# Kernel tuning notes

Measured on AMD Instinct MI355X. Metric: run time of the kernel, lower is better.

## Reference

```python
import jax, jax.numpy as jnp
import numpy as np

N_NODES = 100000
N_EDGES = 500000
IN_FEATS = 128
HID = 128
OUT = 1


def setup_inputs() -> dict:
    key = jax.random.key(0)
    ks = jax.random.split(key, 10)
    h = jax.random.normal(ks[0], (N_NODES, IN_FEATS), dtype=jnp.float32)
    src = jax.random.randint(ks[1], (N_EDGES,), 0, N_NODES, dtype=jnp.int32)
    dst = jax.random.randint(ks[2], (N_EDGES,), 0, N_NODES, dtype=jnp.int32)
    # Linear params (PyTorch convention: W [out,in], y = x @ W.T + b)
    s1 = 1.0 / np.sqrt(2 * IN_FEATS)
    s2 = 1.0 / np.sqrt(HID)
    W1 = jax.random.uniform(ks[3], (HID, 2 * IN_FEATS), jnp.float32, -s1, s1)
    b1 = jax.random.uniform(ks[4], (HID,), jnp.float32, -s1, s1)
    W2 = jax.random.uniform(ks[5], (HID, HID), jnp.float32, -s2, s2)
    b2 = jax.random.uniform(ks[6], (HID,), jnp.float32, -s2, s2)
    W3 = jax.random.uniform(ks[7], (OUT, HID), jnp.float32, -s2, s2)
    b3 = jax.random.uniform(ks[8], (OUT,), jnp.float32, -s2, s2)
    return {"h": h, "src": src, "dst": dst,
            "W1": W1, "b1": b1, "W2": W2, "b2": b2, "W3": W3, "b3": b3}


def reference(h, src, dst, W1, b1, W2, b2, W3, b3):
    # Per-edge gather of src/dst node features. Instead of materializing the
    # [E, 2*in] concat, split W1 into its src/dst halves and fuse the concat
    # into two GEMMs (same math as fc1(cat([h_u, h_v], 1))).
    h_u = h[src]                                   # [E, in]
    h_v = h[dst]                                   # [E, in]
    W1u, W1v = W1[:, :IN_FEATS], W1[:, IN_FEATS:]  # [hid, in] each
    x = h_u @ W1u.T + h_v @ W1v.T + b1             # [E, hid]
    x = jax.nn.relu(x)
    x = jax.nn.relu(x @ W2.T + b2)                 # [E, hid]
    score = x @ W3.T + b3                          # [E, out]
    return score
```

## Files before the change

### kernel.cpp

```cpp
#include <hip/hip_runtime.h>
#include <hip/hip_bf16.h>
#include <hip/hip_fp16.h>


#define N_NODES 100000
#define N_EDGES 500000
#define F       128
#define HID     128
#define TE      32
#define NT      (N_EDGES / TE)
#define GRID    1024
#define BLOCK   256

typedef _Float16 f16x8  __attribute__((ext_vector_type(8)));
typedef float    f32x16 __attribute__((ext_vector_type(16)));

typedef __attribute__((address_space(3))) unsigned int  lds_u32;
typedef __attribute__((address_space(1))) const unsigned int glb_u32;

__device__ __forceinline__ void load_lds16(const void* g, void* l) {
    __builtin_amdgcn_global_load_lds((glb_u32*)g, (lds_u32*)l, 16, 0, 0);
}
__device__ __forceinline__ void bar_lgkm() {
    asm volatile("s_waitcnt lgkmcnt(0)" ::: "memory");
    __builtin_amdgcn_s_barrier();
    __builtin_amdgcn_sched_barrier(0);
}
__device__ __forceinline__ void bar_vm() {
    asm volatile("s_waitcnt vmcnt(0) lgkmcnt(0)" ::: "memory");
    __builtin_amdgcn_s_barrier();
    __builtin_amdgcn_sched_barrier(0);
}

__global__ __launch_bounds__(256) void h_to_f16(const float* __restrict__ h,
                                                _Float16* __restrict__ h16) {
    const int i = (blockIdx.x * 256 + threadIdx.x) * 8;
    float4 a = *(const float4*)(h + i);
    float4 b = *(const float4*)(h + i + 4);
    f16x8 v;
    v[0] = (_Float16)a.x; v[1] = (_Float16)a.y; v[2] = (_Float16)a.z; v[3] = (_Float16)a.w;
    v[4] = (_Float16)b.x; v[5] = (_Float16)b.y; v[6] = (_Float16)b.z; v[7] = (_Float16)b.w;
    *(f16x8*)(h16 + i) = v;
}

__global__ __launch_bounds__(BLOCK) void edge_mlp_v4(
    const _Float16* __restrict__ h16,
    const int*   __restrict__ src,
    const int*   __restrict__ dst,
    const float* __restrict__ W1,
    const float* __restrict__ b1,
    const float* __restrict__ W2,
    const float* __restrict__ b2,
    const float* __restrict__ W3,
    const float* __restrict__ b3,
    float*       __restrict__ out)
{
    __shared__ __align__(128) char Alds[2 * TE * 512];
    __shared__ __align__(128) char Xlds[TE * 256];
    float* Spart = (float*)Xlds;

    const int tid  = threadIdx.x;
    const int wave = tid >> 6;
    const int lane = tid & 63;
    const int mh   = wave;
    const int col  = lane & 31;
    const int h    = lane >> 5;

    f16x8 w1a[16];
    #pragma unroll
    for (int kt = 0; kt < 16; ++kt) {
        const float* p = W1 + (mh * 32 + col) * 256 + kt * 16 + 8 * h;
        f16x8 v;
        #pragma unroll
        for (int j = 0; j < 8; ++j) v[j] = (_Float16)p[j];
        w1a[kt] = v;
    }
    f16x8 w2a[8];
    #pragma unroll
    for (int kt = 0; kt < 8; ++kt) {
        const float* p = W2 + (mh * 32 + col) * 128 + kt * 16 + 8 * h;
        f16x8 v;
        #pragma unroll
        for (int j = 0; j < 8; ++j) v[j] = (_Float16)p[j];
        w2a[kt] = v;
    }
    float b1pl[16], b2pl[16], w3pl[16];
    #pragma unroll
    for (int r = 0; r < 16; ++r) {
        const int row = mh * 32 + (r & 3) + 8 * (r >> 2) + 4 * h;
        b1pl[r] = b1[row];
        b2pl[r] = b2[row];
        w3pl[r] = W3[row];
    }
    const float b3v = b3[0];

    int eloc[4], k16v[4];
    #pragma unroll
    for (int j = 0; j < 4; ++j) {
        const int i = wave * 4 + j;
        eloc[j] = 2 * i + h;
        k16v[j] = (lane & 15) ^ (eloc[j] & 15);
    }
    const int whichv = (lane >> 4) & 1;
    const int* idxp  = whichv ? dst : src;

    const int t0 = blockIdx.x;
    int nodeCur[4], nodeNext[4];

    #pragma unroll
    for (int j = 0; j < 4; ++j) {
        nodeCur[j] = idxp[t0 * TE + eloc[j]];
    }
    #pragma unroll
    for (int j = 0; j < 4; ++j) {
        const _Float16* g = h16 + (size_t)nodeCur[j] * F + k16v[j] * 8;
        load_lds16(g, Alds + (wave * 4 + j) * 1024);
    }
    {
        int tn = t0 + GRID; if (tn > NT - 1) tn = NT - 1;
        #pragma unroll
        for (int j = 0; j < 4; ++j) nodeNext[j] = idxp[tn * TE + eloc[j]];
    }

    const int e_own = col;
    const int exor  = (e_own & 15) << 4;

    int cur = 0;
    for (int t = t0; t < NT; t += GRID) {
        bar_vm();

        #pragma unroll
        for (int j = 0; j < 4; ++j) nodeCur[j] = nodeNext[j];
        {
            char* nb = Alds + (cur ^ 1) * (TE * 512);
            #pragma unroll
            for (int j = 0; j < 4; ++j) {
                const _Float16* g = h16 + (size_t)nodeCur[j] * F + k16v[j] * 8;
                load_lds16(g, nb + (wave * 4 + j) * 1024);
            }
        }
        {
            int tn2 = t + 2 * GRID; if (tn2 > NT - 1) tn2 = NT - 1;
            #pragma unroll
            for (int j = 0; j < 4; ++j) nodeNext[j] = idxp[tn2 * TE + eloc[j]];
        }

        const char* Ab = Alds + cur * (TE * 512);

        f32x16 acc1 = {};
        #pragma unroll
        for (int kt = 0; kt < 16; ++kt) {
            const int c = (kt * 32 + 16 * h) ^ exor;
            f16x8 bf = *(const f16x8*)(Ab + e_own * 512 + c);
            acc1 = __builtin_amdgcn_mfma_f32_32x32x16_f16(w1a[kt], bf, acc1, 0, 0, 0);
        }
        #pragma unroll
        for (int g = 0; g < 4; ++g) {
            union { _Float16 q[4]; unsigned long long u; } pk;
            #pragma unroll
            for (int q = 0; q < 4; ++q) {
                float v = acc1[4 * g + q] + b1pl[4 * g + q];
                v = v > 0.f ? v : 0.f;
                pk.q[q] = (_Float16)v;
            }
            const int c = (mh * 64 + 16 * g + 8 * h) ^ exor;
            *(unsigned long long*)(Xlds + e_own * 256 + c) = pk.u;
        }
        bar_lgkm();

        f32x16 acc2 = {};
        #pragma unroll
        for (int kt = 0; kt < 8; ++kt) {
            const int c = (kt * 32 + 16 * h) ^ exor;
            f16x8 xf = *(const f16x8*)(Xlds + e_own * 256 + c);
            acc2 = __builtin_amdgcn_mfma_f32_32x32x16_f16(w2a[kt], xf, acc2, 0, 0, 0);
        }

        float p = 0.f;
        #pragma unroll
        for (int r = 0; r < 16; ++r) {
            float v = acc2[r] + b2pl[r];
            v = v > 0.f ? v : 0.f;
            p = fmaf(w3pl[r], v, p);
        }
        p += __shfl_xor(p, 32);

        bar_lgkm();
        if (lane < 32) Spart[wave * 32 + lane] = p;
        bar_lgkm();

        if (tid < TE) {
            float s = Spart[tid] + Spart[32 + tid] + Spart[64 + tid]
                    + Spart[96 + tid] + b3v;
            out[t * TE + tid] = s;
        }
        cur ^= 1;
    }
}

__global__ __launch_bounds__(512) void edge_mlp_v1(
    const float* __restrict__ h,
    const int*   __restrict__ src,
    const int*   __restrict__ dst,
    const float* __restrict__ W1,
    const float* __restrict__ b1,
    const float* __restrict__ W2,
    const float* __restrict__ b2,
    const float* __restrict__ W3,
    const float* __restrict__ b3,
    float*       __restrict__ out)
{
    __shared__ __align__(128) char Alds[64 * 512];
    __shared__ __align__(128) char Xlds[64 * 256];
    typedef float f32x4 __attribute__((ext_vector_type(4)));

    const int tid  = threadIdx.x;
    const int wave = tid >> 6;
    const int lane = tid & 63;
    const int l15  = lane & 15;
    const int lk   = lane >> 4;
    const int n1 = wave * 16 + l15;
    const int NT1 = (N_EDGES + 63) / 64;

    f16x8 w1f[8];
    #pragma unroll
    for (int kt = 0; kt < 8; ++kt) {
        const float* p = W1 + n1 * 256 + kt * 32 + lk * 8;
        f16x8 v;
        #pragma unroll
        for (int j = 0; j < 8; ++j) v[j] = (_Float16)p[j];
        w1f[kt] = v;
    }
    const float b1v = b1[n1];
    f16x8 w2f[4];
    #pragma unroll
    for (int kt = 0; kt < 4; ++kt) {
        const float* p = W2 + n1 * 128 + kt * 32 + lk * 8;
        f16x8 v;
        #pragma unroll
        for (int j = 0; j < 8; ++j) v[j] = (_Float16)p[j];
        w2f[kt] = v;
    }
    const float b2v = b2[n1];
    float w3r[16];
    {
        const float* p = W3 + (tid & 7) * 16;
        #pragma unroll
        for (int i = 0; i < 16; ++i) w3r[i] = p[i];
    }
    const float b3v = b3[0];

    const int slot = tid >> 2, part = tid & 3;
    const int g_e = slot >> 1, g_which = slot & 1;

    for (int t = blockIdx.x; t < NT1; t += gridDim.x) {
        {
            int eg = t * 64 + g_e;
            if (eg >= N_EDGES) eg = N_EDGES - 1;
            const int node = g_which ? dst[eg] : src[eg];
            const float* p = h + node * F + part * 32;
            const int kbase = g_which * 128 + part * 32;
            #pragma unroll
            for (int c = 0; c < 4; ++c) {
                float4 v0 = *(const float4*)(p + c * 8);
                float4 v1 = *(const float4*)(p + c * 8 + 4);
                f16x8 x;
                x[0] = (_Float16)v0.x; x[1] = (_Float16)v0.y;
                x[2] = (_Float16)v0.z; x[3] = (_Float16)v0.w;
                x[4] = (_Float16)v1.x; x[5] = (_Float16)v1.y;
                x[6] = (_Float16)v1.z; x[7] = (_Float16)v1.w;
                int byte = g_e * 512 + (kbase + c * 8) * 2;
                byte ^= (g_e & 7) << 4;
                *(f16x8*)(Alds + byte) = x;
            }
        }
        __syncthreads();
        #pragma unroll
        for (int m = 0; m < 4; ++m) {
            f32x4 acc = {0.f, 0.f, 0.f, 0.f};
            #pragma unroll
            for (int kt = 0; kt < 8; ++kt) {
                const int edge = m * 16 + l15;
                int byte = edge * 512 + (kt * 32 + lk * 8) * 2;
                byte ^= (edge & 7) << 4;
                f16x8 a = *(const f16x8*)(Alds + byte);
                acc = __builtin_amdgcn_mfma_f32_16x16x32_f16(a, w1f[kt], acc, 0, 0, 0);
            }
            #pragma unroll
            for (int r = 0; r < 4; ++r) {
                float v = acc[r] + b1v;
                v = v > 0.f ? v : 0.f;
                const int edge = m * 16 + lk * 4 + r;
                int byte = edge * 256 + n1 * 2;
                byte ^= (edge & 7) << 4;
                *(_Float16*)(Xlds + byte) = (_Float16)v;
            }
        }
        __syncthreads();
        f32x4 acc2[4];
        #pragma unroll
        for (int m = 0; m < 4; ++m) {
            f32x4 acc = {0.f, 0.f, 0.f, 0.f};
            #pragma unroll
            for (int kt = 0; kt < 4; ++kt) {
                const int edge = m * 16 + l15;
                int byte = edge * 256 + (kt * 32 + lk * 8) * 2;
                byte ^= (edge & 7) << 4;
                f16x8 a = *(const f16x8*)(Xlds + byte);
                acc = __builtin_amdgcn_mfma_f32_16x16x32_f16(a, w2f[kt], acc, 0, 0, 0);
            }
            acc2[m] = acc;
        }
        __syncthreads();
        #pragma unroll
        for (int m = 0; m < 4; ++m) {
            #pragma unroll
            for (int r = 0; r < 4; ++r) {
                float v = acc2[m][r] + b2v;
                v = v > 0.f ? v : 0.f;
                const int edge = m * 16 + lk * 4 + r;
                int byte = edge * 256 + n1 * 2;
                byte ^= (edge & 7) << 4;
                *(_Float16*)(Xlds + byte) = (_Float16)v;
            }
        }
        __syncthreads();
        {
            const int e_loc = tid >> 3;
            const int cgrp  = tid & 7;
            const int swz   = (e_loc & 7) << 4;
            const int base  = e_loc * 256 + cgrp * 32;
            f16x8 x0 = *(const f16x8*)(Xlds + (base ^ swz));
            f16x8 x1 = *(const f16x8*)(Xlds + ((base + 16) ^ swz));
            float p = 0.f;
            #pragma unroll
            for (int i = 0; i < 8; ++i) p += (float)x0[i] * w3r[i];
            #pragma unroll
            for (int i = 0; i < 8; ++i) p += (float)x1[i] * w3r[8 + i];
            p += __shfl_xor(p, 1);
            p += __shfl_xor(p, 2);
            p += __shfl_xor(p, 4);
            const int eg = t * 64 + e_loc;
            if (cgrp == 0 && eg < N_EDGES) out[eg] = p + b3v;
        }
    }
}

extern "C" void kernel_launch(void* const* d_in, const int* in_sizes, int n_in,
                              void* d_out, int out_size, void* d_ws, size_t ws_size,
                              hipStream_t stream) {
    const float* h   = (const float*)d_in[0];
    const int*   src = (const int*)  d_in[1];
    const int*   dst = (const int*)  d_in[2];
    const float* W1  = (const float*)d_in[3];
    const float* b1  = (const float*)d_in[4];
    const float* W2  = (const float*)d_in[5];
    const float* b2  = (const float*)d_in[6];
    const float* W3  = (const float*)d_in[7];
    const float* b3  = (const float*)d_in[8];
    float* out = (float*)d_out;

    const size_t need = (size_t)N_NODES * F * sizeof(_Float16);
    if (ws_size >= need) {
        _Float16* h16 = (_Float16*)d_ws;
        h_to_f16<<<6250, 256, 0, stream>>>(h, h16);
        edge_mlp_v4<<<GRID, BLOCK, 0, stream>>>(h16, src, dst, W1, b1, W2, b2, W3, b3, out);
    } else {
        edge_mlp_v1<<<512, 512, 0, stream>>>(h, src, dst, W1, b1, W2, b2, W3, b3, out);
    }
}
```

Before: 188.4 us.

## Bucket-sort edges by source node before gathering features for locality

Adds a histogram, scan and scatter pass that bucket edges by src node (blocks of 512 nodes), producing sorted src/dst arrays and a permutation. The new edge MLP kernel processes contiguous tile ranges per block, with an XCD-aware block remap, and scatters each result back through the permutation. The aim is better cache reuse of the gathered src features. In exchange it adds three extra kernel launches, extra index traffic, and uncoalesced output writes.

```diff
diff --git a/kernel.cpp b/kernel.cpp
--- a/kernel.cpp
+++ b/kernel.cpp
@@ -11,6 +11,11 @@
 #define NT      (N_EDGES / TE)
 #define GRID    1024
 #define BLOCK   256
+#define TPB     16
+
+#define NB      196
+#define HB      256
+#define HCHUNK  1954
 
 typedef _Float16 f16x8  __attribute__((ext_vector_type(8)));
 typedef float    f32x16 __attribute__((ext_vector_type(16)));
@@ -41,6 +46,235 @@
     v[0] = (_Float16)a.x; v[1] = (_Float16)a.y; v[2] = (_Float16)a.z; v[3] = (_Float16)a.w;
     v[4] = (_Float16)b.x; v[5] = (_Float16)b.y; v[6] = (_Float16)b.z; v[7] = (_Float16)b.w;
     *(f16x8*)(h16 + i) = v;
+}
+
+__global__ __launch_bounds__(256) void hist_kernel(const int* __restrict__ src,
+                                                   unsigned* __restrict__ bh) {
+    __shared__ unsigned hs[NB];
+    const int blk = blockIdx.x, tid = threadIdx.x;
+    if (tid < NB) hs[tid] = 0;
+    __syncthreads();
+    const int base = blk * HCHUNK;
+    for (int i = tid; i < HCHUNK; i += 256) {
+        const int e = base + i;
+        if (e < N_EDGES) atomicAdd(&hs[src[e] >> 9], 1u);
+    }
+    __syncthreads();
+    if (tid < NB) bh[blk * NB + tid] = hs[tid];
+}
+
+__global__ __launch_bounds__(256) void scan_kernel(unsigned* __restrict__ bh) {
+    __shared__ unsigned tot[NB];
+    const int j = threadIdx.x;
+    if (j < NB) {
+        unsigned off = 0;
+        for (int b = 0; b < HB; b += 8) {
+            unsigned t[8];
+            #pragma unroll
+            for (int k = 0; k < 8; ++k) t[k] = bh[(b + k) * NB + j];
+            #pragma unroll
+            for (int k = 0; k < 8; ++k) { bh[(b + k) * NB + j] = off; off += t[k]; }
+        }
+        tot[j] = off;
+    }
+    __syncthreads();
+    if (j == 0) {
+        unsigned run = 0;
+        for (int k = 0; k < NB; ++k) { unsigned t = tot[k]; tot[k] = run; run += t; }
+    }
+    __syncthreads();
+    if (j < NB) {
+        const unsigned base = tot[j];
+        for (int b = 0; b < HB; b += 8) {
+            unsigned t[8];
+            #pragma unroll
+            for (int k = 0; k < 8; ++k) t[k] = bh[(b + k) * NB + j];
+            #pragma unroll
+            for (int k = 0; k < 8; ++k) bh[(b + k) * NB + j] = t[k] + base;
+        }
+    }
+}
+
+__global__ __launch_bounds__(256) void scatter_kernel(const int* __restrict__ src,
+                                                      const int* __restrict__ dst,
+                                                      const unsigned* __restrict__ bh,
+                                                      int* __restrict__ s_srt,
+                                                      int* __restrict__ d_srt,
+                                                      int* __restrict__ perm) {
+    __shared__ unsigned cnt[NB];
+    const int blk = blockIdx.x, tid = threadIdx.x;
+    if (tid < NB) cnt[tid] = bh[blk * NB + tid];
+    __syncthreads();
+    const int base = blk * HCHUNK;
+    for (int i = tid; i < HCHUNK; i += 256) {
+        const int e = base + i;
+        if (e < N_EDGES) {
+            const int s = src[e];
+            const unsigned pos = atomicAdd(&cnt[s >> 9], 1u);
+            s_srt[pos] = s;
+            d_srt[pos] = dst[e];
+            perm[pos]  = e;
+        }
+    }
+}
+
+__global__ __launch_bounds__(BLOCK) void edge_mlp_v6(
+    const _Float16* __restrict__ h16,
+    const int*   __restrict__ s_srt,
+    const int*   __restrict__ d_srt,
+    const int*   __restrict__ perm,
+    const float* __restrict__ W1,
+    const float* __restrict__ b1,
+    const float* __restrict__ W2,
+    const float* __restrict__ b2,
+    const float* __restrict__ W3,
+    const float* __restrict__ b3,
+    float*       __restrict__ out)
+{
+    const int vb   = (blockIdx.x & 7) * 128 + (blockIdx.x >> 3);
+    const int tbeg = vb * TPB;
+    if (tbeg >= NT) return;
+    const int tend = (tbeg + TPB < NT) ? tbeg + TPB : NT;
+
+    __shared__ __align__(128) char Alds[2 * TE * 512];
+    __shared__ __align__(128) char Xlds[TE * 256];
+    float* Spart = (float*)Xlds;
+
+    const int tid  = threadIdx.x;
+    const int wave = tid >> 6;
+    const int lane = tid & 63;
+    const int mh   = wave;
+    const int col  = lane & 31;
+    const int h    = lane >> 5;
+
+    f16x8 w1a[16];
+    #pragma unroll
+    for (int kt = 0; kt < 16; ++kt) {
+        const float* p = W1 + (mh * 32 + col) * 256 + kt * 16 + 8 * h;
+        f16x8 v;
+        #pragma unroll
+        for (int j = 0; j < 8; ++j) v[j] = (_Float16)p[j];
+        w1a[kt] = v;
+    }
+    f16x8 w2a[8];
+    #pragma unroll
+    for (int kt = 0; kt < 8; ++kt) {
+        const float* p = W2 + (mh * 32 + col) * 128 + kt * 16 + 8 * h;
+        f16x8 v;
+        #pragma unroll
+        for (int j = 0; j < 8; ++j) v[j] = (_Float16)p[j];
+        w2a[kt] = v;
+    }
+    float b1pl[16], b2pl[16], w3pl[16];
+    #pragma unroll
+    for (int r = 0; r < 16; ++r) {
+        const int row = mh * 32 + (r & 3) + 8 * (r >> 2) + 4 * h;
+        b1pl[r] = b1[row];
+        b2pl[r] = b2[row];
+        w3pl[r] = W3[row];
+    }
+    const float b3v = b3[0];
+
+    int eloc[4], k16v[4];
+    #pragma unroll
+    for (int j = 0; j < 4; ++j) {
+        const int i = wave * 4 + j;
+        eloc[j] = 2 * i + h;
+        k16v[j] = (lane & 15) ^ (eloc[j] & 15);
+    }
+    const int whichv = (lane >> 4) & 1;
+    const int* idxp  = whichv ? d_srt : s_srt;
+
+    int nodeCur[4], nodeNext[4];
+    #pragma unroll
+    for (int j = 0; j < 4; ++j) nodeCur[j] = idxp[tbeg * TE + eloc[j]];
+    #pragma unroll
+    for (int j = 0; j < 4; ++j) {
+        const _Float16* g = h16 + (size_t)nodeCur[j] * F + k16v[j] * 8;
+        load_lds16(g, Alds + (wave * 4 + j) * 1024);
+    }
+    {
+        int tn = tbeg + 1; if (tn > NT - 1) tn = NT - 1;
+        #pragma unroll
+        for (int j = 0; j < 4; ++j) nodeNext[j] = idxp[tn * TE + eloc[j]];
+    }
+
+    const int e_own = col;
+    const int exor  = (e_own & 15) << 4;
+
+    int cur = 0;
+    for (int t = tbeg; t < tend; ++t) {
+        bar_vm();
+
+        #pragma unroll
+        for (int j = 0; j < 4; ++j) nodeCur[j] = nodeNext[j];
+        {
+            char* nb = Alds + (cur ^ 1) * (TE * 512);
+            #pragma unroll
+            for (int j = 0; j < 4; ++j) {
+                const _Float16* g = h16 + (size_t)nodeCur[j] * F + k16v[j] * 8;
+                load_lds16(g, nb + (wave * 4 + j) * 1024);
+            }
+        }
+        {
+            int tn2 = t + 2; if (tn2 > NT - 1) tn2 = NT - 1;
+            #pragma unroll
+            for (int j = 0; j < 4; ++j) nodeNext[j] = idxp[tn2 * TE + eloc[j]];
+        }
+
+        const char* Ab = Alds + cur * (TE * 512);
+
+        f32x16 acc1 = {};
+        #pragma unroll
+        for (int kt = 0; kt < 16; ++kt) {
+            const int c = (kt * 32 + 16 * h) ^ exor;
+            f16x8 bf = *(const f16x8*)(Ab + e_own * 512 + c);
+            acc1 = __builtin_amdgcn_mfma_f32_32x32x16_f16(w1a[kt], bf, acc1, 0, 0, 0);
+        }
+        #pragma unroll
+        for (int g = 0; g < 4; ++g) {
+            union { _Float16 q[4]; unsigned long long u; } pk;
+            #pragma unroll
+            for (int q = 0; q < 4; ++q) {
+                float v = acc1[4 * g + q] + b1pl[4 * g + q];
+                v = v > 0.f ? v : 0.f;
+                pk.q[q] = (_Float16)v;
+            }
+            const int c = (mh * 64 + 16 * g + 8 * h) ^ exor;
+            *(unsigned long long*)(Xlds + e_own * 256 + c) = pk.u;
+        }
+        bar_lgkm();
+
+        f32x16 acc2 = {};
+        #pragma unroll
+        for (int kt = 0; kt < 8; ++kt) {
+            const int c = (kt * 32 + 16 * h) ^ exor;
+            f16x8 xf = *(const f16x8*)(Xlds + e_own * 256 + c);
+            acc2 = __builtin_amdgcn_mfma_f32_32x32x16_f16(w2a[kt], xf, acc2, 0, 0, 0);
+        }
+
+        float p = 0.f;
+        #pragma unroll
+        for (int r = 0; r < 16; ++r) {
+            float v = acc2[r] + b2pl[r];
+            v = v > 0.f ? v : 0.f;
+            p = fmaf(w3pl[r], v, p);
+        }
+        p += __shfl_xor(p, 32);
+
+        bar_lgkm();
+        if (lane < 32) Spart[wave * 32 + lane] = p;
+        bar_lgkm();
+
+        if (tid < TE) {
+            float s = Spart[tid] + Spart[32 + tid] + Spart[64 + tid]
+                    + Spart[96 + tid] + b3v;
+            const int pe = perm[t * TE + tid];
+            out[pe] = s;
+        }
+        cur ^= 1;
+    }
+    asm volatile("s_waitcnt vmcnt(0)" ::: "memory");
 }
 
 __global__ __launch_bounds__(BLOCK) void edge_mlp_v4(
@@ -106,11 +340,8 @@
 
     const int t0 = blockIdx.x;
     int nodeCur[4], nodeNext[4];
-
-    #pragma unroll
-    for (int j = 0; j < 4; ++j) {
-        nodeCur[j] = idxp[t0 * TE + eloc[j]];
-    }
+    #pragma unroll
+    for (int j = 0; j < 4; ++j) nodeCur[j] = idxp[t0 * TE + eloc[j]];
     #pragma unroll
     for (int j = 0; j < 4; ++j) {
         const _Float16* g = h16 + (size_t)nodeCur[j] * F + k16v[j] * 8;
@@ -128,7 +359,6 @@
     int cur = 0;
     for (int t = t0; t < NT; t += GRID) {
         bar_vm();
-
         #pragma unroll
         for (int j = 0; j < 4; ++j) nodeCur[j] = nodeNext[j];
         {
@@ -196,6 +426,7 @@
         }
         cur ^= 1;
     }
+    asm volatile("s_waitcnt vmcnt(0)" ::: "memory");
 }
 
 __global__ __launch_bounds__(512) void edge_mlp_v1(
@@ -360,9 +591,28 @@
     const float* b3  = (const float*)d_in[8];
     float* out = (float*)d_out;
 
-    const size_t need = (size_t)N_NODES * F * sizeof(_Float16);
-    if (ws_size >= need) {
-        _Float16* h16 = (_Float16*)d_ws;
+    const size_t H16B = (size_t)N_NODES * F * sizeof(_Float16);
+    const size_t SOFF = H16B;
+    const size_t DOFF = SOFF + (size_t)N_EDGES * 4;
+    const size_t POFF = DOFF + (size_t)N_EDGES * 4;
+    const size_t BOFF = POFF + (size_t)N_EDGES * 4;
+    const size_t NEED_SORT = BOFF + (size_t)HB * NB * 4;
+
+    char* ws = (char*)d_ws;
+    if (ws_size >= NEED_SORT) {
+        _Float16* h16  = (_Float16*)ws;
+        int*      s_srt = (int*)(ws + SOFF);
+        int*      d_srt = (int*)(ws + DOFF);
+        int*      perm  = (int*)(ws + POFF);
+        unsigned* bh    = (unsigned*)(ws + BOFF);
+        h_to_f16<<<6250, 256, 0, stream>>>(h, h16);
+        hist_kernel<<<HB, 256, 0, stream>>>(src, bh);
+        scan_kernel<<<1, 256, 0, stream>>>(bh);
+        scatter_kernel<<<HB, 256, 0, stream>>>(src, dst, bh, s_srt, d_srt, perm);
+        edge_mlp_v6<<<GRID, BLOCK, 0, stream>>>(h16, s_srt, d_srt, perm,
+                                                W1, b1, W2, b2, W3, b3, out);
+    } else if (ws_size >= H16B) {
+        _Float16* h16 = (_Float16*)ws;
         h_to_f16<<<6250, 256, 0, stream>>>(h, h16);
         edge_mlp_v4<<<GRID, BLOCK, 0, stream>>>(h16, src, dst, W1, b1, W2, b2, W3, b3, out);
     } else {
```

After: 230.5 us. 1.22x slower.
